# Kernel optimization log

Measured on AMD Instinct MI355X. Metric: run time of the kernel, lower is better.

Reference implementation:

```python
import jax, jax.numpy as jnp
import numpy as np
from jax import lax

BN_EPS = 1e-5


def binarize(v):
    """Sign binarization with clipped straight-through estimator.
    Forward: sign(v). Backward: grad * 1{|v| <= 1} (hardtanh STE), matching
    the standard 1w1a BinaryFunction used in XNOR/IR-Net style repos."""
    clipped = jnp.clip(v, -1.0, 1.0)
    return clipped + lax.stop_gradient(jnp.sign(v) - clipped)


def setup_inputs() -> dict:
    key = jax.random.key(0)
    k1, k2, k3, k4 = jax.random.split(key, 4)
    x = jax.random.normal(k1, (32, 256, 56, 56), dtype=jnp.float32)
    w = jax.random.normal(k2, (256, 256, 3, 3), dtype=jnp.float32) * 0.05
    gamma = jax.random.uniform(k3, (256,), dtype=jnp.float32, minval=0.5, maxval=1.5)
    beta = jax.random.normal(k4, (256,), dtype=jnp.float32) * 0.1
    return {"x": x, "w": w, "gamma": gamma, "beta": beta}


def reference(x, w, gamma, beta):
    # Binarize activations and weights (1-bit each) -> XNOR-style conv in FP math.
    bx = binarize(x)                       # [N, C_in, H, W] in {-1, 0, +1}
    bw = binarize(w)                       # [C_out, C_in, kH, kW]
    y = lax.conv_general_dilated(
        bx, bw,
        window_strides=(1, 1),
        padding=((1, 1), (1, 1)),
        dimension_numbers=("NCHW", "OIHW", "NCHW"),
    )                                      # [N, C_out, H, W]
    # BatchNorm2d in training mode: batch statistics over N, H, W per channel.
    mean = jnp.mean(y, axis=(0, 2, 3))
    var = jnp.var(y, axis=(0, 2, 3))
    inv = lax.rsqrt(var + BN_EPS)
    out = (y - mean[None, :, None, None]) * (gamma * inv)[None, :, None, None] \
        + beta[None, :, None, None]
    return out
```

## Files before the change

### kernel.cpp

```cpp
#include <hip/hip_runtime.h>
#include <stdint.h>

typedef unsigned long long u64;
typedef unsigned int u32;
typedef int v4i  __attribute__((ext_vector_type(4)));
typedef int v16i __attribute__((ext_vector_type(16)));

#define N_IMG 32
#define C_IN  256
#define C_OUT 256
#define H     56
#define W     56
#define HW    (H*W)
#define NHW   (N_IMG*HW)
#define CHW   (C_IN*HW)

#define PX_BYTES  3211264
#define WPK_BYTES 589824
#define Y_OFF     (PX_BYTES + WPK_BYTES)

__global__ __launch_bounds__(256)
void pack_x_kernel(const float* __restrict__ x, u64* __restrict__ px) {
    int t = blockIdx.x * 256 + threadIdx.x;
    int w4   = t % 14;
    int r    = t / 14;
    int word = r & 3;
    int r2   = r >> 2;
    int h    = r2 % H;
    int n    = r2 / H;
    const float4* src = (const float4*)(x + ((size_t)(n*C_IN + word*64) * HW + h*W + w4*4));
    u64 b0 = 0, b1 = 0, b2 = 0, b3 = 0;
    #pragma unroll 8
    for (int j = 0; j < 64; ++j) {
        float4 v = src[(size_t)j * (HW/4)];
        b0 |= (u64)(__float_as_uint(v.x) >> 31) << j;
        b1 |= (u64)(__float_as_uint(v.y) >> 31) << j;
        b2 |= (u64)(__float_as_uint(v.z) >> 31) << j;
        b3 |= (u64)(__float_as_uint(v.w) >> 31) << j;
    }
    u64* dst = px + (((size_t)((n*H + h)*W + w4*4)) << 2) + word;
    dst[0] = b0; dst[4] = b1; dst[8] = b2; dst[12] = b3;
}

__global__ __launch_bounds__(256)
void pack_wpk_kernel(const float* __restrict__ wt, char* __restrict__ wpk) {
    int t = blockIdx.x * 256 + threadIdx.x;
    int co = t & 255;
    int tk = t >> 8;
    int tap = tk >> 3;
    int kb  = tk & 7;
    u32* out = (u32*)wpk + t*8;
    #pragma unroll
    for (int g = 0; g < 8; ++g) {
        u32 dw = 0;
        #pragma unroll
        for (int b = 0; b < 4; ++b) {
            int ci = kb*32 + 4*g + b;
            float v = wt[((size_t)(co*C_IN + ci)) * 9 + tap];
            u32 byte = (__float_as_uint(v) >> 31) ? 0xFFu : 0x01u;
            dw |= byte << (8*b);
        }
        out[g] = dw;
    }
}

__global__ __launch_bounds__(256, 2)
void conv_mfma_kernel(const u64* __restrict__ px, const char* __restrict__ wpk,
                      short* __restrict__ y) {
    __shared__ char lds[4*66*256];
    int bx = blockIdx.x;
    int n  = bx / 28;
    int h0 = (bx % 28) * 2;
    int cobase = blockIdx.y * 128;
    int tid = threadIdx.x;

    for (int i = tid; i < 4*66; i += 256) {
        int row = i / 66;
        int wp  = i % 66;
        int hh = h0 + row - 1;
        int ww = wp - 1;
        bool valid = ((unsigned)hh < (unsigned)H) && ((unsigned)ww < (unsigned)W);
        u64 wv0 = 0, wv1 = 0, wv2 = 0, wv3 = 0;
        if (valid) {
            const u64* s = px + (((size_t)((n*H + hh)*W + ww)) << 2);
            wv0 = s[0]; wv1 = s[1]; wv2 = s[2]; wv3 = s[3];
        }
        u32 basev = valid ? 0x01010101u : 0u;
        char* out = lds + i*256;
        int sw = (wp & 15) << 4;
        u64 wvs[4] = {wv0, wv1, wv2, wv3};
        #pragma unroll
        for (int c4 = 0; c4 < 16; ++c4) {
            u32 bits = (u32)(wvs[c4>>2] >> ((c4&3)*16)) & 0xFFFFu;
            v4i ov;
            #pragma unroll
            for (int d = 0; d < 4; ++d) {
                u32 sel = (bits >> (4*d)) & 0xFu;
                u32 sp  = (sel * 0x204081u) & 0x01010101u;
                u32 m   = (sp << 8) - (sp << 1);
                ov[d] = (int)(basev + m);
            }
            *(v4i*)(out + ((c4*16) ^ sw)) = ov;
        }
    }
    __syncthreads();

    int wid  = tid >> 6;
    int lane = tid & 63;
    int l31  = lane & 31;
    int lhalf = lane >> 5;
    int lh16 = lhalf << 4;
    int cot  = cobase + wid*32;

    int p1 = 32 + l31, p3 = 96 + l31;
    int hr1 = (p1 >= 56);
    int wl0 = l31;
    int wl1 = p1 - (hr1 ? 56 : 0);
    int wl2 = (64 + l31) - 56;
    int wl3a = p3 - 56; int wl3 = wl3a > 55 ? 55 : wl3a;
    int rb0 = 0, rb1 = hr1 * (66*256), rb2 = 66*256, rb3 = 66*256;

    v16i acc0 = {0,0,0,0,0,0,0,0,0,0,0,0,0,0,0,0};
    v16i acc1 = acc0, acc2 = acc0, acc3 = acc0;

    const v4i* wq = (const v4i*)wpk;

    #pragma unroll
    for (int tap = 0; tap < 9; ++tap) {
        const int dw  = tap % 3;
        const int rof = (tap / 3) * (66*256);
        int wp0 = wl0 + dw, wp1 = wl1 + dw, wp2 = wl2 + dw, wp3 = wl3 + dw;
        int sw0 = (wp0 & 15) << 4, sw1 = (wp1 & 15) << 4;
        int sw2 = (wp2 & 15) << 4, sw3 = (wp3 & 15) << 4;
        int a0 = rb0 + rof + wp0*256;
        int a1 = rb1 + rof + wp1*256;
        int a2 = rb2 + rof + wp2*256;
        int a3 = rb3 + rof + wp3*256;
        #pragma unroll
        for (int kb = 0; kb < 8; ++kb) {
            v4i av = wq[(((tap*8 + kb)*256 + cot + l31) << 1) | lhalf];
            int kof = kb*32 + lh16;
            v4i b0 = *(const v4i*)(lds + a0 + (kof ^ sw0));
            v4i b1 = *(const v4i*)(lds + a1 + (kof ^ sw1));
            v4i b2 = *(const v4i*)(lds + a2 + (kof ^ sw2));
            v4i b3 = *(const v4i*)(lds + a3 + (kof ^ sw3));
            acc0 = __builtin_amdgcn_mfma_i32_32x32x32_i8(av, b0, acc0, 0, 0, 0);
            acc1 = __builtin_amdgcn_mfma_i32_32x32x32_i8(av, b1, acc1, 0, 0, 0);
            acc2 = __builtin_amdgcn_mfma_i32_32x32x32_i8(av, b2, acc2, 0, 0, 0);
            acc3 = __builtin_amdgcn_mfma_i32_32x32x32_i8(av, b3, acc3, 0, 0, 0);
        }
    }

    size_t ybase = (size_t)n*CHW + (size_t)(cot + (lhalf << 2))*HW;
    {
        size_t o = ybase + (size_t)(h0 + 0)*W + wl0;
        #pragma unroll
        for (int rg = 0; rg < 16; ++rg)
            y[o + (size_t)((rg&3) + 8*(rg>>2))*HW] = (short)acc0[rg];
    }
    {
        size_t o = ybase + (size_t)(h0 + hr1)*W + wl1;
        #pragma unroll
        for (int rg = 0; rg < 16; ++rg)
            y[o + (size_t)((rg&3) + 8*(rg>>2))*HW] = (short)acc1[rg];
    }
    {
        size_t o = ybase + (size_t)(h0 + 1)*W + wl2;
        #pragma unroll
        for (int rg = 0; rg < 16; ++rg)
            y[o + (size_t)((rg&3) + 8*(rg>>2))*HW] = (short)acc2[rg];
    }
    if (l31 < 16) {
        size_t o = ybase + (size_t)(h0 + 1)*W + wl3;
        #pragma unroll
        for (int rg = 0; rg < 16; ++rg)
            y[o + (size_t)((rg&3) + 8*(rg>>2))*HW] = (short)acc3[rg];
    }
}

__global__ __launch_bounds__(256)
void stats_kernel(const short* __restrict__ y, long long* __restrict__ partials) {
    int slab = blockIdx.x;
    const int4* ys = (const int4*)(y + (size_t)slab * HW);
    int s = 0, sq = 0;
    for (int i = threadIdx.x; i < HW/8; i += 256) {
        int4 v = ys[i];
        int vv[4] = {v.x, v.y, v.z, v.w};
        #pragma unroll
        for (int k = 0; k < 4; ++k) {
            int lo = (short)(vv[k] & 0xFFFF);
            int hi = (short)(vv[k] >> 16);
            s  += lo + hi;
            sq += lo*lo + hi*hi;
        }
    }
    __shared__ int       rs[256];
    __shared__ long long rq[256];
    rs[threadIdx.x] = s;
    rq[threadIdx.x] = sq;
    __syncthreads();
    for (int off = 128; off > 0; off >>= 1) {
        if (threadIdx.x < off) {
            rs[threadIdx.x] += rs[threadIdx.x + off];
            rq[threadIdx.x] += rq[threadIdx.x + off];
        }
        __syncthreads();
    }
    if (threadIdx.x == 0) {
        partials[2*slab]   = rs[0];
        partials[2*slab+1] = rq[0];
    }
}

__global__ __launch_bounds__(256)
void apply_kernel(const short* __restrict__ y, const long long* __restrict__ partials,
                  const float* __restrict__ gamma, const float* __restrict__ beta,
                  float* __restrict__ out) {
    int slab = blockIdx.x;
    int co = slab & 255;
    long long S = 0, SS = 0;
    #pragma unroll 8
    for (int m = 0; m < N_IMG; ++m) {
        S  += partials[2*((m<<8) | co)];
        SS += partials[2*((m<<8) | co) + 1];
    }
    double mean = (double)S  * (1.0 / (double)NHW);
    double var  = (double)SS * (1.0 / (double)NHW) - mean*mean;
    float a = gamma[co] * rsqrtf((float)var + 1e-5f);
    float b = beta[co] - (float)mean * a;

    const int4* ys = (const int4*)(y + (size_t)slab * HW);
    float4*     os = (float4*)(out + (size_t)slab * HW);
    for (int i = threadIdx.x; i < HW/8; i += 256) {
        int4 v = ys[i];
        float4 f0, f1;
        f0.x = a * (float)((short)(v.x & 0xFFFF)) + b;
        f0.y = a * (float)((short)(v.x >> 16))    + b;
        f0.z = a * (float)((short)(v.y & 0xFFFF)) + b;
        f0.w = a * (float)((short)(v.y >> 16))    + b;
        f1.x = a * (float)((short)(v.z & 0xFFFF)) + b;
        f1.y = a * (float)((short)(v.z >> 16))    + b;
        f1.z = a * (float)((short)(v.w & 0xFFFF)) + b;
        f1.w = a * (float)((short)(v.w >> 16))    + b;
        os[2*i]   = f0;
        os[2*i+1] = f1;
    }
}

extern "C" void kernel_launch(void* const* d_in, const int* in_sizes, int n_in,
                              void* d_out, int out_size, void* d_ws, size_t ws_size,
                              hipStream_t stream) {
    const float* x     = (const float*)d_in[0];
    const float* wt    = (const float*)d_in[1];
    const float* gamma = (const float*)d_in[2];
    const float* beta  = (const float*)d_in[3];
    float* out = (float*)d_out;

    char* ws = (char*)d_ws;
    u64*   px  = (u64*)ws;
    char*  wpk = ws + PX_BYTES;
    short* y   = (short*)(ws + Y_OFF);
    long long* partials = (long long*)ws;

    hipLaunchKernelGGL(pack_x_kernel,   dim3(100352/256), dim3(256), 0, stream, x, px);
    hipLaunchKernelGGL(pack_wpk_kernel, dim3(72),         dim3(256), 0, stream, wt, wpk);
    hipLaunchKernelGGL(conv_mfma_kernel,dim3(896, 2),     dim3(256), 0, stream, px, wpk, y);
    hipLaunchKernelGGL(stats_kernel,    dim3(8192),       dim3(256), 0, stream, y, partials);
    hipLaunchKernelGGL(apply_kernel,    dim3(8192),       dim3(256), 0, stream, y, partials, gamma, beta, out);
}
```

Baseline: 319.3 us.

## Retile conv waves to 2x2 MFMA blocks over channels and pixels

Each wave now computes a 64-output-channel by 64-pixel block (two weight fragments times two pixel fragments) instead of 32 channels by 128 pixels. This halves the LDS activation reads per MFMA and raises reuse of each loaded fragment from 1:4 to 2:2, at the cost of doubling the global weight loads per wave. The wave-to-work mapping is split into a channel quarter and a pixel half, and the stores are rearranged to match.

```diff
diff --git a/kernel.cpp b/kernel.cpp
--- a/kernel.cpp
+++ b/kernel.cpp
@@ -105,23 +105,28 @@
     }
     __syncthreads();
 
-    int wid  = tid >> 6;
-    int lane = tid & 63;
-    int l31  = lane & 31;
+    int wid   = tid >> 6;
+    int lane  = tid & 63;
+    int l31   = lane & 31;
     int lhalf = lane >> 5;
-    int lh16 = lhalf << 4;
-    int cot  = cobase + wid*32;
-
-    int p1 = 32 + l31, p3 = 96 + l31;
-    int hr1 = (p1 >= 56);
-    int wl0 = l31;
-    int wl1 = p1 - (hr1 ? 56 : 0);
-    int wl2 = (64 + l31) - 56;
-    int wl3a = p3 - 56; int wl3 = wl3a > 55 ? 55 : wl3a;
-    int rb0 = 0, rb1 = hr1 * (66*256), rb2 = 66*256, rb3 = 66*256;
-
-    v16i acc0 = {0,0,0,0,0,0,0,0,0,0,0,0,0,0,0,0};
-    v16i acc1 = acc0, acc2 = acc0, acc3 = acc0;
+    int lh16  = lhalf << 4;
+    int coq   = wid & 1;
+    int pxh   = wid >> 1;
+    int cot   = cobase + coq*64;
+
+    int pj0 = pxh*64 + l31;
+    int pj1 = pj0 + 32;
+    int r0 = (pj0 >= 56) ? 1 : 0;
+    int w0 = pj0 - 56*r0;
+    int r1 = (pj1 >= 56) ? 1 : 0;
+    int w1 = pj1 - 56*r1; if (w1 > 55) w1 = 55;
+    int rb0 = r0 * (66*256);
+    int rb1 = r1 * (66*256);
+
+    v16i acc00 = {0,0,0,0,0,0,0,0,0,0,0,0,0,0,0,0};
+    v16i acc01 = acc00;
+    v16i acc10 = acc00;
+    v16i acc11 = acc00;
 
     const v4i* wq = (const v4i*)wpk;
 
@@ -129,52 +134,50 @@
     for (int tap = 0; tap < 9; ++tap) {
         const int dw  = tap % 3;
         const int rof = (tap / 3) * (66*256);
-        int wp0 = wl0 + dw, wp1 = wl1 + dw, wp2 = wl2 + dw, wp3 = wl3 + dw;
+        int wp0 = w0 + dw, wp1 = w1 + dw;
         int sw0 = (wp0 & 15) << 4, sw1 = (wp1 & 15) << 4;
-        int sw2 = (wp2 & 15) << 4, sw3 = (wp3 & 15) << 4;
         int a0 = rb0 + rof + wp0*256;
         int a1 = rb1 + rof + wp1*256;
-        int a2 = rb2 + rof + wp2*256;
-        int a3 = rb3 + rof + wp3*256;
         #pragma unroll
         for (int kb = 0; kb < 8; ++kb) {
-            v4i av = wq[(((tap*8 + kb)*256 + cot + l31) << 1) | lhalf];
+            int widx = ((tap*8 + kb)*256 + cot + l31) << 1;
+            v4i av0 = wq[widx | lhalf];
+            v4i av1 = wq[(widx + 64) | lhalf];
             int kof = kb*32 + lh16;
             v4i b0 = *(const v4i*)(lds + a0 + (kof ^ sw0));
             v4i b1 = *(const v4i*)(lds + a1 + (kof ^ sw1));
-            v4i b2 = *(const v4i*)(lds + a2 + (kof ^ sw2));
-            v4i b3 = *(const v4i*)(lds + a3 + (kof ^ sw3));
-            acc0 = __builtin_amdgcn_mfma_i32_32x32x32_i8(av, b0, acc0, 0, 0, 0);
-            acc1 = __builtin_amdgcn_mfma_i32_32x32x32_i8(av, b1, acc1, 0, 0, 0);
-            acc2 = __builtin_amdgcn_mfma_i32_32x32x32_i8(av, b2, acc2, 0, 0, 0);
-            acc3 = __builtin_amdgcn_mfma_i32_32x32x32_i8(av, b3, acc3, 0, 0, 0);
-        }
-    }
-
-    size_t ybase = (size_t)n*CHW + (size_t)(cot + (lhalf << 2))*HW;
+            acc00 = __builtin_amdgcn_mfma_i32_32x32x32_i8(av0, b0, acc00, 0, 0, 0);
+            acc01 = __builtin_amdgcn_mfma_i32_32x32x32_i8(av0, b1, acc01, 0, 0, 0);
+            acc10 = __builtin_amdgcn_mfma_i32_32x32x32_i8(av1, b0, acc10, 0, 0, 0);
+            acc11 = __builtin_amdgcn_mfma_i32_32x32x32_i8(av1, b1, acc11, 0, 0, 0);
+        }
+    }
+
+    size_t yb0 = (size_t)n*CHW + (size_t)(cot + (lhalf << 2))*HW;
+    size_t yb1 = yb0 + (size_t)32*HW;
+    int hr0 = h0 + r0, hr1 = h0 + r1;
+    bool full1 = !(pxh == 1 && l31 >= 16);
     {
-        size_t o = ybase + (size_t)(h0 + 0)*W + wl0;
-        #pragma unroll
-        for (int rg = 0; rg < 16; ++rg)
-            y[o + (size_t)((rg&3) + 8*(rg>>2))*HW] = (short)acc0[rg];
+        size_t o = yb0 + (size_t)hr0*W + w0;
+        #pragma unroll
+        for (int rg = 0; rg < 16; ++rg)
+            y[o + (size_t)((rg&3) + 8*(rg>>2))*HW] = (short)acc00[rg];
     }
     {
-        size_t o = ybase + (size_t)(h0 + hr1)*W + wl1;
-        #pragma unroll
-        for (int rg = 0; rg < 16; ++rg)
-            y[o + (size_t)((rg&3) + 8*(rg>>2))*HW] = (short)acc1[rg];
-    }
-    {
-        size_t o = ybase + (size_t)(h0 + 1)*W + wl2;
-        #pragma unroll
-        for (int rg = 0; rg < 16; ++rg)
-            y[o + (size_t)((rg&3) + 8*(rg>>2))*HW] = (short)acc2[rg];
-    }
-    if (l31 < 16) {
-        size_t o = ybase + (size_t)(h0 + 1)*W + wl3;
-        #pragma unroll
-        for (int rg = 0; rg < 16; ++rg)
-            y[o + (size_t)((rg&3) + 8*(rg>>2))*HW] = (short)acc3[rg];
+        size_t o = yb1 + (size_t)hr0*W + w0;
+        #pragma unroll
+        for (int rg = 0; rg < 16; ++rg)
+            y[o + (size_t)((rg&3) + 8*(rg>>2))*HW] = (short)acc10[rg];
+    }
+    if (full1) {
+        size_t o = yb0 + (size_t)hr1*W + w1;
+        #pragma unroll
+        for (int rg = 0; rg < 16; ++rg)
+            y[o + (size_t)((rg&3) + 8*(rg>>2))*HW] = (short)acc01[rg];
+        o = yb1 + (size_t)hr1*W + w1;
+        #pragma unroll
+        for (int rg = 0; rg < 16; ++rg)
+            y[o + (size_t)((rg&3) + 8*(rg>>2))*HW] = (short)acc11[rg];
     }
 }
 
```

Measured after the change: 363.3 us. +13.8%, slower.
